# Kernel optimization log

Measured on AMD Instinct MI355X. Metric: run time of the kernel, lower is better.

Reference implementation:

```python
import jax, jax.numpy as jnp
import numpy as np

N = 100000
FEAT = 256
HID = 128
OUT = 64
E = 1600000


def setup_inputs() -> dict:
    key = jax.random.key(0)
    ks = jax.random.split(key, 8)
    x = jax.random.normal(ks[0], (N, FEAT), dtype=jnp.float32)
    edge_index = jax.random.randint(ks[1], (2, E), 0, N, dtype=jnp.int64)
    # Glorot-like weights, zero bias (PyG GCNConv default init style)
    def glorot(k, fin, fout):
        s = (6.0 / (fin + fout)) ** 0.5
        return jax.random.uniform(k, (fin, fout), jnp.float32, -s, s)
    return {
        "x": x,
        "edge_index": edge_index,
        "W1": glorot(ks[2], FEAT, HID), "b1": jnp.zeros((HID,), jnp.float32),
        "W2": glorot(ks[3], HID, HID), "b2": jnp.zeros((HID,), jnp.float32),
        "W3": glorot(ks[4], HID, OUT), "b3": jnp.zeros((OUT,), jnp.float32),
    }


def _gcn_prep(edge_index, n_nodes):
    # Add self-loops and compute symmetric normalization deg^-1/2 (PyG gcn_norm).
    loops = jnp.arange(n_nodes, dtype=edge_index.dtype)
    src = jnp.concatenate([edge_index[0], loops])
    dst = jnp.concatenate([edge_index[1], loops])
    ones = jnp.ones(src.shape[0], dtype=jnp.float32)
    deg = jax.ops.segment_sum(ones, dst, num_segments=n_nodes)
    dinv = jnp.where(deg > 0, jax.lax.rsqrt(jnp.maximum(deg, 1.0)), 0.0)
    norm = dinv[src] * dinv[dst]  # [E+N]
    return src, dst, norm


def _gcn_layer(x, src, dst, norm, W, b, n_nodes):
    h = x @ W                              # [N, F_out]
    msg = h[src] * norm[:, None]           # gather + edge scale
    out = jax.ops.segment_sum(msg, dst, num_segments=n_nodes)  # scatter-add
    return out + b


def reference(x, edge_index, W1, b1, W2, b2, W3, b3):
    n = x.shape[0]
    src, dst, norm = _gcn_prep(edge_index, n)
    h = jax.nn.relu(_gcn_layer(x, src, dst, norm, W1, b1, n))
    h = jax.nn.relu(_gcn_layer(h, src, dst, norm, W2, b2, n))
    return _gcn_layer(h, src, dst, norm, W3, b3, n)
```

## Files before the change

kernel.cpp:

```cpp
#include <hip/hip_runtime.h>
#include <hip/hip_bf16.h>


#define NNODES 100000
#define NB 391
#define PB 2048
#define BCAP 12288

typedef _Float16 half8  __attribute__((ext_vector_type(8)));
typedef _Float16 half4v __attribute__((ext_vector_type(4)));
typedef _Float16 half2v __attribute__((ext_vector_type(2)));
typedef float    floatx4 __attribute__((ext_vector_type(4)));

static __device__ __forceinline__ floatx4 h2f4(half4v v) {
    return (floatx4){(float)v.x, (float)v.y, (float)v.z, (float)v.w};
}

__global__ __launch_bounds__(256) void blockhist_k(const int* __restrict__ dst,
                                                   int* __restrict__ H, int e) {
    __shared__ int h[NB];
    for (int q = threadIdx.x; q < NB; q += 256) h[q] = 0;
    __syncthreads();
    int base = blockIdx.x * PB;
    int lim = e - base; if (lim > PB) lim = PB;
    for (int i = threadIdx.x; i < lim; i += 256)
        atomicAdd(&h[dst[base + i] >> 8], 1);
    __syncthreads();
    for (int q = threadIdx.x; q < NB; q += 256)
        H[(size_t)blockIdx.x * NB + q] = h[q];
}

__global__ __launch_bounds__(256) void bucketscan_k(const int* __restrict__ H,
                                                    int* __restrict__ O,
                                                    int* __restrict__ T, int npb) {
    __shared__ int lds[256];
    int b = blockIdx.x, t = threadIdx.x;
    int running = 0;
    for (int c0 = 0; c0 < npb; c0 += 256) {
        int idx = c0 + t;
        int v = (idx < npb) ? H[(size_t)idx * NB + b] : 0;
        lds[t] = v;
        __syncthreads();
        #pragma unroll
        for (int off = 1; off < 256; off <<= 1) {
            int u = (t >= off) ? lds[t - off] : 0;
            __syncthreads();
            lds[t] += u;
            __syncthreads();
        }
        int excl = lds[t] - v + running;
        if (idx < npb) O[(size_t)idx * NB + b] = excl;
        running += lds[255];
        __syncthreads();
    }
    if (t == 0) T[b] = running;
}

__global__ __launch_bounds__(512) void scanT_k(const int* __restrict__ T,
                                               int* __restrict__ bbase, int e) {
    __shared__ int lds[512];
    int t = threadIdx.x;
    int v = (t < NB) ? T[t] : 0;
    lds[t] = v;
    __syncthreads();
    #pragma unroll
    for (int off = 1; off < 512; off <<= 1) {
        int u = (t >= off) ? lds[t - off] : 0;
        __syncthreads();
        lds[t] += u;
        __syncthreads();
    }
    if (t < NB) bbase[t] = lds[t] - v;
    if (t == 0) bbase[NB] = e;
}

__global__ __launch_bounds__(256) void scatter_k(const int* __restrict__ src,
                                                 const int* __restrict__ dst,
                                                 const int* __restrict__ O,
                                                 const int* __restrict__ bbase,
                                                 unsigned* __restrict__ binned, int e) {
    __shared__ int cur[NB];
    for (int q = threadIdx.x; q < NB; q += 256)
        cur[q] = bbase[q] + O[(size_t)blockIdx.x * NB + q];
    __syncthreads();
    int base = blockIdx.x * PB;
    int lim = e - base; if (lim > PB) lim = PB;
    for (int i = threadIdx.x; i < lim; i += 256) {
        int d = dst[base + i];
        int s = src[base + i];
        int p = atomicAdd(&cur[d >> 8], 1);
        binned[p] = ((unsigned)(d & 255) << 17) | (unsigned)s;
    }
}

__global__ __launch_bounds__(256) void bucket_fill_k(
    const unsigned* __restrict__ binned, const int* __restrict__ bbase,
    int* __restrict__ rowptr, int* __restrict__ eidx,
    float* __restrict__ dinv, int n, int e) {
    __shared__ int cnt[256];
    __shared__ int cur[256];
    __shared__ int lds[256];
    __shared__ int sbuf[BCAP];
    int b = blockIdx.x, t = threadIdx.x;
    int beg = bbase[b], end = bbase[b + 1];
    int m = end - beg;
    cnt[t] = 0;
    __syncthreads();
    for (int q = t; q < m; q += 256) {
        unsigned r = binned[beg + q];
        atomicAdd(&cnt[r >> 17], 1);
    }
    __syncthreads();
    int v = cnt[t];
    lds[t] = v;
    __syncthreads();
    #pragma unroll
    for (int off = 1; off < 256; off <<= 1) {
        int u = (t >= off) ? lds[t - off] : 0;
        __syncthreads();
        lds[t] += u;
        __syncthreads();
    }
    int excl = lds[t] - v;
    int node = b * 256 + t;
    if (node < n) {
        rowptr[node] = beg + excl;
        dinv[node] = rsqrtf(1.0f + (float)v);
    }
    if (b == NB - 1 && t == 0) rowptr[n] = e;
    cur[t] = excl;
    __syncthreads();
    for (int q = t; q < m; q += 256) {
        unsigned r = binned[beg + q];
        int p = atomicAdd(&cur[r >> 17], 1);
        if (p < BCAP) sbuf[p] = (int)(r & 0x1FFFFu);
    }
    __syncthreads();
    for (int q = t; q < m; q += 256) eidx[beg + q] = sbuf[q];
}

static __device__ __forceinline__ void cast_frag(
    const float* __restrict__ W, _Float16* __restrict__ Wf,
    int FIN, int FOUT, int i) {
    int k = i / FOUT, n = i % FOUT;
    int ct = n >> 4, mrow = n & 15;
    int kc = k >> 5, hi = (k & 31) >> 3, j = k & 7;
    int NKC = FIN / 32;
    int idx = ((ct * NKC + kc) * 64 + hi * 16 + mrow) * 8 + j;
    Wf[idx] = (_Float16)W[(size_t)k * FOUT + n];
}

__global__ __launch_bounds__(256) void castW_k(
    const float* __restrict__ W1, const float* __restrict__ W2,
    const float* __restrict__ W3, _Float16* __restrict__ Wf1,
    _Float16* __restrict__ Wf2, _Float16* __restrict__ Wf3) {
    int i = blockIdx.x * 256 + threadIdx.x;
    if (i < 256 * 128) cast_frag(W1, Wf1, 256, 128, i);
    if (i < 128 * 128) cast_frag(W2, Wf2, 128, 128, i);
    if (i < 128 * 64)  cast_frag(W3, Wf3, 128, 64, i);
}

template<typename TA, int FIN, int FOUT>
__global__ __launch_bounds__(256, 2) void gemm_ldsB_k(
    const TA* __restrict__ X, const _Float16* __restrict__ Wf,
    const float* __restrict__ dinv, _Float16* __restrict__ G, int n)
{
    constexpr int NKC = FIN / 32;
    constexpr int NCT = FOUT / 16;
    __shared__ _Float16 wS[FOUT * FIN];

    const int tid  = threadIdx.x;
    const int wave = tid >> 6;
    const int lane = tid & 63;
    const int mrow = lane & 15;
    const int kq   = (lane >> 4) * 8;

    {
        const half8* s = (const half8*)Wf;
        half8* d = (half8*)wS;
        constexpr int TOT8 = FOUT * FIN / 8;
        #pragma unroll
        for (int i = tid; i < TOT8; i += 256) d[i] = s[i];
    }

    int r = blockIdx.x * 64 + wave * 16 + mrow;
    if (r > n - 1) r = n - 1;

    half8 af[NKC];
    if constexpr (sizeof(TA) == 4) {
        const float* xp = (const float*)X + (size_t)r * FIN + kq;
        float4 t0[NKC], t1[NKC];
        #pragma unroll
        for (int kc = 0; kc < NKC; ++kc) {
            t0[kc] = *(const float4*)(xp + kc * 32);
            t1[kc] = *(const float4*)(xp + kc * 32 + 4);
        }
        #pragma unroll
        for (int kc = 0; kc < NKC; ++kc) {
            float4 u0 = t0[kc], u1 = t1[kc];
            af[kc] = (half8){(_Float16)u0.x, (_Float16)u0.y, (_Float16)u0.z, (_Float16)u0.w,
                             (_Float16)u1.x, (_Float16)u1.y, (_Float16)u1.z, (_Float16)u1.w};
        }
    } else {
        const _Float16* xp = (const _Float16*)X + (size_t)r * FIN + kq;
        #pragma unroll
        for (int kc = 0; kc < NKC; ++kc)
            af[kc] = *(const half8*)(xp + kc * 32);
    }

    __syncthreads();

    floatx4 acc[NCT];
    #pragma unroll
    for (int ct = 0; ct < NCT; ++ct) acc[ct] = (floatx4){0.f, 0.f, 0.f, 0.f};

    #pragma unroll
    for (int kc = 0; kc < NKC; ++kc) {
        #pragma unroll
        for (int ct = 0; ct < NCT; ++ct) {
            half8 bf = *(const half8*)&wS[(((ct * NKC) + kc) * 64 + lane) * 8];
            acc[ct] = __builtin_amdgcn_mfma_f32_16x16x32_f16(af[kc], bf, acc[ct], 0, 0, 0);
        }
    }

    int rbase = blockIdx.x * 64 + wave * 16 + (lane >> 4) * 4;
    #pragma unroll
    for (int reg = 0; reg < 4; ++reg) {
        int rr = rbase + reg;
        if (rr < n) {
            float s = dinv[rr];
            #pragma unroll
            for (int ct = 0; ct < NCT; ++ct)
                G[(size_t)rr * FOUT + ct * 16 + mrow] = (_Float16)(acc[ct][reg] * s);
        }
    }
}

template<bool RELU, typename OutT>
__global__ __launch_bounds__(256) void gather128_k(
    const _Float16* __restrict__ g, const int* __restrict__ rowptr,
    const int* __restrict__ eidx, const float* __restrict__ dinv,
    const float* __restrict__ bias, OutT* __restrict__ out, int n)
{
    int wave = threadIdx.x >> 6;
    int lane = threadIdx.x & 63;
    int half = lane >> 5;
    int hl   = lane & 31;
    int node = blockIdx.x * 4 + wave;
    if (node >= n) return;

    int beg = rowptr[node];
    int end = rowptr[node + 1];

    const half4v* g4 = (const half4v*)g;
    floatx4 aA = {0.f,0.f,0.f,0.f}, aB = aA, aC = aA, aD = aA;
    if (half == 0) aA = h2f4(g4[(size_t)node * 32 + hl]);

    for (int j0 = beg; j0 < end; j0 += 64) {
        int m = end - j0; if (m > 64) m = 64;
        int id = (lane < m) ? eidx[j0 + lane] : 0;
        int t = 0;
        for (; t + 7 < m; t += 8) {
            int i0 = __shfl(id, t + half);
            int i1 = __shfl(id, t + 2 + half);
            int i2 = __shfl(id, t + 4 + half);
            int i3 = __shfl(id, t + 6 + half);
            half4v v0 = g4[(size_t)i0 * 32 + hl];
            half4v v1 = g4[(size_t)i1 * 32 + hl];
            half4v v2 = g4[(size_t)i2 * 32 + hl];
            half4v v3 = g4[(size_t)i3 * 32 + hl];
            aA += h2f4(v0); aB += h2f4(v1); aC += h2f4(v2); aD += h2f4(v3);
        }
        for (; t + 1 < m; t += 2) {
            int i0 = __shfl(id, t + half);
            aA += h2f4(g4[(size_t)i0 * 32 + hl]);
        }
        if (t < m) {
            int i0 = __shfl(id, t);
            if (half == 0) aA += h2f4(g4[(size_t)i0 * 32 + hl]);
        }
    }
    aA += aB; aC += aD; aA += aC;
    aA.x += __shfl_down(aA.x, 32);
    aA.y += __shfl_down(aA.y, 32);
    aA.z += __shfl_down(aA.z, 32);
    aA.w += __shfl_down(aA.w, 32);

    if (half == 0) {
        float sc = dinv[node];
        float4 bb = *(const float4*)(bias + 4 * hl);
        float o0 = fmaf(aA.x, sc, bb.x);
        float o1 = fmaf(aA.y, sc, bb.y);
        float o2 = fmaf(aA.z, sc, bb.z);
        float o3 = fmaf(aA.w, sc, bb.w);
        if (RELU) {
            o0 = fmaxf(o0, 0.f); o1 = fmaxf(o1, 0.f);
            o2 = fmaxf(o2, 0.f); o3 = fmaxf(o3, 0.f);
        }
        if constexpr (sizeof(OutT) == 2) {
            ((half4v*)out)[(size_t)node * 32 + hl] =
                (half4v){(_Float16)o0, (_Float16)o1, (_Float16)o2, (_Float16)o3};
        } else {
            *(float4*)((float*)out + (size_t)node * 128 + 4 * hl) =
                make_float4(o0, o1, o2, o3);
        }
    }
}

template<bool RELU>
__global__ __launch_bounds__(256) void gather64_k(
    const _Float16* __restrict__ g, const int* __restrict__ rowptr,
    const int* __restrict__ eidx, const float* __restrict__ dinv,
    const float* __restrict__ bias, float* __restrict__ out, int n)
{
    int wave = threadIdx.x >> 6;
    int lane = threadIdx.x & 63;
    int half = lane >> 5;
    int hl   = lane & 31;
    int node = blockIdx.x * 4 + wave;
    if (node >= n) return;

    int beg = rowptr[node];
    int end = rowptr[node + 1];

    const half2v* g2 = (const half2v*)g;
    float ax=0.f, ay=0.f, bx=0.f, by=0.f, cx=0.f, cy=0.f, dx=0.f, dy=0.f;
    if (half == 0) {
        half2v v = g2[(size_t)node * 32 + hl];
        ax = (float)v.x; ay = (float)v.y;
    }

    for (int j0 = beg; j0 < end; j0 += 64) {
        int m = end - j0; if (m > 64) m = 64;
        int id = (lane < m) ? eidx[j0 + lane] : 0;
        int t = 0;
        for (; t + 7 < m; t += 8) {
            int i0 = __shfl(id, t + half);
            int i1 = __shfl(id, t + 2 + half);
            int i2 = __shfl(id, t + 4 + half);
            int i3 = __shfl(id, t + 6 + half);
            half2v v0 = g2[(size_t)i0 * 32 + hl];
            half2v v1 = g2[(size_t)i1 * 32 + hl];
            half2v v2 = g2[(size_t)i2 * 32 + hl];
            half2v v3 = g2[(size_t)i3 * 32 + hl];
            ax += (float)v0.x; ay += (float)v0.y;
            bx += (float)v1.x; by += (float)v1.y;
            cx += (float)v2.x; cy += (float)v2.y;
            dx += (float)v3.x; dy += (float)v3.y;
        }
        for (; t + 1 < m; t += 2) {
            int i0 = __shfl(id, t + half);
            half2v v0 = g2[(size_t)i0 * 32 + hl];
            ax += (float)v0.x; ay += (float)v0.y;
        }
        if (t < m) {
            int i0 = __shfl(id, t);
            if (half == 0) {
                half2v v0 = g2[(size_t)i0 * 32 + hl];
                ax += (float)v0.x; ay += (float)v0.y;
            }
        }
    }
    ax += bx + cx + dx; ay += by + cy + dy;
    ax += __shfl_down(ax, 32);
    ay += __shfl_down(ay, 32);

    if (half == 0) {
        float sc = dinv[node];
        float2 bb = *(const float2*)(bias + 2 * hl);
        float ox = fmaf(ax, sc, bb.x);
        float oy = fmaf(ay, sc, bb.y);
        if (RELU) { ox = fmaxf(ox, 0.f); oy = fmaxf(oy, 0.f); }
        *(float2*)(out + (size_t)node * 64 + 2 * hl) = make_float2(ox, oy);
    }
}

extern "C" void kernel_launch(void* const* d_in, const int* in_sizes, int n_in,
                              void* d_out, int out_size, void* d_ws, size_t ws_size,
                              hipStream_t stream) {
    const float* x  = (const float*)d_in[0];
    const int*   ei = (const int*)d_in[1];
    const float* W1 = (const float*)d_in[2];
    const float* b1 = (const float*)d_in[3];
    const float* W2 = (const float*)d_in[4];
    const float* b2 = (const float*)d_in[5];
    const float* W3 = (const float*)d_in[6];
    const float* b3 = (const float*)d_in[7];
    float* out = (float*)d_out;

    const int N = NNODES;
    const int E = in_sizes[1] / 2;
    const int* srcI = ei;
    const int* dstI = ei + E;

    const int npb = (E + PB - 1) / PB;

    char* ws = (char*)d_ws;
    size_t p = 0;
    auto alloc = [&](size_t bytes) { void* r = ws + p; p = (p + bytes + 255) & ~(size_t)255; return r; };
    float*     dinv   = (float*)    alloc((size_t)N * 4);
    int*       rowptr = (int*)      alloc((size_t)(N + 1) * 4);
    int*       bbase  = (int*)      alloc((size_t)(NB + 1) * 4);
    int*       T      = (int*)      alloc((size_t)NB * 4);
    int*       H      = (int*)      alloc((size_t)npb * NB * 4);
    int*       O      = (int*)      alloc((size_t)npb * NB * 4);
    unsigned*  binned = (unsigned*) alloc((size_t)E * 4);
    int*       eidx   = (int*)      alloc((size_t)E * 4);
    _Float16*  Wf1    = (_Float16*) alloc((size_t)128 * 256 * 2);
    _Float16*  Wf2    = (_Float16*) alloc((size_t)128 * 128 * 2);
    _Float16*  Wf3    = (_Float16*) alloc((size_t)64 * 128 * 2);
    _Float16*  A      = (_Float16*) alloc((size_t)N * 128 * 2);
    _Float16*  Ch     = (_Float16*) alloc((size_t)N * 128 * 2);

    const int nb_node4 = (N + 3) / 4;
    const int nb_gemm = (N + 63) / 64;

    blockhist_k<<<npb, 256, 0, stream>>>(dstI, H, E);
    castW_k<<<128, 256, 0, stream>>>(W1, W2, W3, Wf1, Wf2, Wf3);
    bucketscan_k<<<NB, 256, 0, stream>>>(H, O, T, npb);
    scanT_k<<<1, 512, 0, stream>>>(T, bbase, E);
    scatter_k<<<npb, 256, 0, stream>>>(srcI, dstI, O, bbase, binned, E);
    bucket_fill_k<<<NB, 256, 0, stream>>>(binned, bbase, rowptr, eidx, dinv, N, E);

    gemm_ldsB_k<float, 256, 128><<<nb_gemm, 256, 0, stream>>>(x, Wf1, dinv, A, N);
    gather128_k<true, _Float16><<<nb_node4, 256, 0, stream>>>(A, rowptr, eidx, dinv, b1, Ch, N);

    gemm_ldsB_k<_Float16, 128, 128><<<nb_gemm, 256, 0, stream>>>(Ch, Wf2, dinv, A, N);
    gather128_k<true, _Float16><<<nb_node4, 256, 0, stream>>>(A, rowptr, eidx, dinv, b2, Ch, N);

    gemm_ldsB_k<_Float16, 128, 64><<<nb_gemm, 256, 0, stream>>>(Ch, Wf3, dinv, A, N);
    gather64_k<false><<<nb_node4, 256, 0, stream>>>(A, rowptr, eidx, dinv, b3, out, N);
}
```

Measured before the change: 445.3 us.

## Store features in 16-column chunk-major layout and gather per chunk

The GEMM output and the gather input/output switch from row-major to a chunk-major layout, with 16 half-precision columns per chunk and every node contiguous within a chunk. Each gather block handles a single chunk, so the working set of gathered rows (N×32 bytes) is small enough to stay cache-resident across random neighbour accesses. A quarter-wave now processes one node, loading 16 edge indices at a time and reducing with xor shuffles. In exchange, edge indices and rowptr are read once per chunk (8×) instead of once in total, and partial edge batches waste lanes.

```diff
diff --git a/kernel.cpp b/kernel.cpp
--- a/kernel.cpp
+++ b/kernel.cpp
@@ -9,7 +9,6 @@
 
 typedef _Float16 half8  __attribute__((ext_vector_type(8)));
 typedef _Float16 half4v __attribute__((ext_vector_type(4)));
-typedef _Float16 half2v __attribute__((ext_vector_type(2)));
 typedef float    floatx4 __attribute__((ext_vector_type(4)));
 
 static __device__ __forceinline__ floatx4 h2f4(half4v v) {
@@ -202,10 +201,12 @@
                              (_Float16)u1.x, (_Float16)u1.y, (_Float16)u1.z, (_Float16)u1.w};
         }
     } else {
-        const _Float16* xp = (const _Float16*)X + (size_t)r * FIN + kq;
-        #pragma unroll
-        for (int kc = 0; kc < NKC; ++kc)
-            af[kc] = *(const half8*)(xp + kc * 32);
+        const _Float16* xp = (const _Float16*)X;
+        #pragma unroll
+        for (int kc = 0; kc < NKC; ++kc) {
+            int f0 = kc * 32 + kq;
+            af[kc] = *(const half8*)(xp + ((size_t)(f0 >> 4) * n + r) * 16 + (f0 & 15));
+        }
     }
 
     __syncthreads();
@@ -231,147 +232,89 @@
             float s = dinv[rr];
             #pragma unroll
             for (int ct = 0; ct < NCT; ++ct)
-                G[(size_t)rr * FOUT + ct * 16 + mrow] = (_Float16)(acc[ct][reg] * s);
-        }
-    }
-}
-
-template<bool RELU, typename OutT>
-__global__ __launch_bounds__(256) void gather128_k(
+                G[((size_t)ct * n + rr) * 16 + mrow] = (_Float16)(acc[ct][reg] * s);
+        }
+    }
+}
+
+template<int NCHUNK, bool RELU, bool F32OUT>
+__global__ __launch_bounds__(256) void gatherchunk_k(
     const _Float16* __restrict__ g, const int* __restrict__ rowptr,
     const int* __restrict__ eidx, const float* __restrict__ dinv,
-    const float* __restrict__ bias, OutT* __restrict__ out, int n)
+    const float* __restrict__ bias, void* __restrict__ outv, int n)
 {
-    int wave = threadIdx.x >> 6;
-    int lane = threadIdx.x & 63;
-    int half = lane >> 5;
-    int hl   = lane & 31;
-    int node = blockIdx.x * 4 + wave;
-    if (node >= n) return;
-
-    int beg = rowptr[node];
-    int end = rowptr[node + 1];
-
-    const half4v* g4 = (const half4v*)g;
-    floatx4 aA = {0.f,0.f,0.f,0.f}, aB = aA, aC = aA, aD = aA;
-    if (half == 0) aA = h2f4(g4[(size_t)node * 32 + hl]);
-
-    for (int j0 = beg; j0 < end; j0 += 64) {
-        int m = end - j0; if (m > 64) m = 64;
-        int id = (lane < m) ? eidx[j0 + lane] : 0;
-        int t = 0;
-        for (; t + 7 < m; t += 8) {
-            int i0 = __shfl(id, t + half);
-            int i1 = __shfl(id, t + 2 + half);
-            int i2 = __shfl(id, t + 4 + half);
-            int i3 = __shfl(id, t + 6 + half);
-            half4v v0 = g4[(size_t)i0 * 32 + hl];
-            half4v v1 = g4[(size_t)i1 * 32 + hl];
-            half4v v2 = g4[(size_t)i2 * 32 + hl];
-            half4v v3 = g4[(size_t)i3 * 32 + hl];
-            aA += h2f4(v0); aB += h2f4(v1); aC += h2f4(v2); aD += h2f4(v3);
-        }
-        for (; t + 1 < m; t += 2) {
-            int i0 = __shfl(id, t + half);
-            aA += h2f4(g4[(size_t)i0 * 32 + hl]);
-        }
-        if (t < m) {
-            int i0 = __shfl(id, t);
-            if (half == 0) aA += h2f4(g4[(size_t)i0 * 32 + hl]);
-        }
-    }
-    aA += aB; aC += aD; aA += aC;
-    aA.x += __shfl_down(aA.x, 32);
-    aA.y += __shfl_down(aA.y, 32);
-    aA.z += __shfl_down(aA.z, 32);
-    aA.w += __shfl_down(aA.w, 32);
-
-    if (half == 0) {
-        float sc = dinv[node];
-        float4 bb = *(const float4*)(bias + 4 * hl);
-        float o0 = fmaf(aA.x, sc, bb.x);
-        float o1 = fmaf(aA.y, sc, bb.y);
-        float o2 = fmaf(aA.z, sc, bb.z);
-        float o3 = fmaf(aA.w, sc, bb.w);
+    const int lane    = threadIdx.x & 63;
+    const int wave    = threadIdx.x >> 6;
+    const int quarter = lane >> 4;
+    const int ql      = lane & 15;
+    const int grp     = ql >> 2;
+    const int q       = ql & 3;
+
+    const int cg = blockIdx.x & 7;
+    const int nb = blockIdx.x >> 3;
+    int chunk, n0, nlim;
+    if constexpr (NCHUNK == 8) {
+        chunk = cg; n0 = 0; nlim = n;
+    } else {
+        chunk = cg & 3;
+        int hh = (n + 1) >> 1;
+        n0   = (cg >> 2) ? hh : 0;
+        nlim = (cg >> 2) ? n  : hh;
+    }
+    const _Float16* __restrict__ gc = g + (size_t)chunk * n * 16;
+    const float4 bb = *(const float4*)(bias + chunk * 16 + 4 * q);
+
+    const int node = n0 + nb * 16 + wave * 4 + quarter;
+    if (node >= nlim) return;
+
+    const int beg = rowptr[node];
+    const int end = rowptr[node + 1];
+    const float sc = dinv[node];
+
+    floatx4 acc = {0.f, 0.f, 0.f, 0.f};
+    {
+        half4v v = *(const half4v*)(gc + ((node << 4) | (q << 2)));
+        if (grp == 0) acc = h2f4(v);
+    }
+
+    for (int j0 = beg; j0 < end; j0 += 16) {
+        int m = end - j0; if (m > 16) m = 16;
+        int id = (ql < m) ? __builtin_nontemporal_load(eidx + j0 + ql) : 0;
+        #pragma unroll
+        for (int t = 0; t < 16; t += 4) {
+            int e = t + grp;
+            int src = __shfl(id, (lane & 48) + e);
+            half4v v = *(const half4v*)(gc + ((src << 4) | (q << 2)));
+            if (e < m) acc += h2f4(v);
+        }
+    }
+
+    #pragma unroll
+    for (int off = 4; off <= 8; off <<= 1) {
+        acc.x += __shfl_xor(acc.x, off);
+        acc.y += __shfl_xor(acc.y, off);
+        acc.z += __shfl_xor(acc.z, off);
+        acc.w += __shfl_xor(acc.w, off);
+    }
+
+    if (grp == 0) {
+        float o0 = fmaf(acc.x, sc, bb.x);
+        float o1 = fmaf(acc.y, sc, bb.y);
+        float o2 = fmaf(acc.z, sc, bb.z);
+        float o3 = fmaf(acc.w, sc, bb.w);
         if (RELU) {
             o0 = fmaxf(o0, 0.f); o1 = fmaxf(o1, 0.f);
             o2 = fmaxf(o2, 0.f); o3 = fmaxf(o3, 0.f);
         }
-        if constexpr (sizeof(OutT) == 2) {
-            ((half4v*)out)[(size_t)node * 32 + hl] =
-                (half4v){(_Float16)o0, (_Float16)o1, (_Float16)o2, (_Float16)o3};
+        if constexpr (F32OUT) {
+            floatx4* p = (floatx4*)((float*)outv + (size_t)node * (NCHUNK * 16)
+                                    + chunk * 16 + 4 * q);
+            __builtin_nontemporal_store((floatx4){o0, o1, o2, o3}, p);
         } else {
-            *(float4*)((float*)out + (size_t)node * 128 + 4 * hl) =
-                make_float4(o0, o1, o2, o3);
-        }
-    }
-}
-
-template<bool RELU>
-__global__ __launch_bounds__(256) void gather64_k(
-    const _Float16* __restrict__ g, const int* __restrict__ rowptr,
-    const int* __restrict__ eidx, const float* __restrict__ dinv,
-    const float* __restrict__ bias, float* __restrict__ out, int n)
-{
-    int wave = threadIdx.x >> 6;
-    int lane = threadIdx.x & 63;
-    int half = lane >> 5;
-    int hl   = lane & 31;
-    int node = blockIdx.x * 4 + wave;
-    if (node >= n) return;
-
-    int beg = rowptr[node];
-    int end = rowptr[node + 1];
-
-    const half2v* g2 = (const half2v*)g;
-    float ax=0.f, ay=0.f, bx=0.f, by=0.f, cx=0.f, cy=0.f, dx=0.f, dy=0.f;
-    if (half == 0) {
-        half2v v = g2[(size_t)node * 32 + hl];
-        ax = (float)v.x; ay = (float)v.y;
-    }
-
-    for (int j0 = beg; j0 < end; j0 += 64) {
-        int m = end - j0; if (m > 64) m = 64;
-        int id = (lane < m) ? eidx[j0 + lane] : 0;
-        int t = 0;
-        for (; t + 7 < m; t += 8) {
-            int i0 = __shfl(id, t + half);
-            int i1 = __shfl(id, t + 2 + half);
-            int i2 = __shfl(id, t + 4 + half);
-            int i3 = __shfl(id, t + 6 + half);
-            half2v v0 = g2[(size_t)i0 * 32 + hl];
-            half2v v1 = g2[(size_t)i1 * 32 + hl];
-            half2v v2 = g2[(size_t)i2 * 32 + hl];
-            half2v v3 = g2[(size_t)i3 * 32 + hl];
-            ax += (float)v0.x; ay += (float)v0.y;
-            bx += (float)v1.x; by += (float)v1.y;
-            cx += (float)v2.x; cy += (float)v2.y;
-            dx += (float)v3.x; dy += (float)v3.y;
-        }
-        for (; t + 1 < m; t += 2) {
-            int i0 = __shfl(id, t + half);
-            half2v v0 = g2[(size_t)i0 * 32 + hl];
-            ax += (float)v0.x; ay += (float)v0.y;
-        }
-        if (t < m) {
-            int i0 = __shfl(id, t);
-            if (half == 0) {
-                half2v v0 = g2[(size_t)i0 * 32 + hl];
-                ax += (float)v0.x; ay += (float)v0.y;
-            }
-        }
-    }
-    ax += bx + cx + dx; ay += by + cy + dy;
-    ax += __shfl_down(ax, 32);
-    ay += __shfl_down(ay, 32);
-
-    if (half == 0) {
-        float sc = dinv[node];
-        float2 bb = *(const float2*)(bias + 2 * hl);
-        float ox = fmaf(ax, sc, bb.x);
-        float oy = fmaf(ay, sc, bb.y);
-        if (RELU) { ox = fmaxf(ox, 0.f); oy = fmaxf(oy, 0.f); }
-        *(float2*)(out + (size_t)node * 64 + 2 * hl) = make_float2(ox, oy);
+            half4v hv = {(_Float16)o0, (_Float16)o1, (_Float16)o2, (_Float16)o3};
+            half4v* p = (half4v*)outv + ((size_t)chunk * n + node) * 4 + q;
+            __builtin_nontemporal_store(hv, p);
+        }
     }
 }
 
@@ -412,8 +355,9 @@
     _Float16*  A      = (_Float16*) alloc((size_t)N * 128 * 2);
     _Float16*  Ch     = (_Float16*) alloc((size_t)N * 128 * 2);
 
-    const int nb_node4 = (N + 3) / 4;
-    const int nb_gemm = (N + 63) / 64;
+    const int nb_gemm  = (N + 63) / 64;
+    const int nb_gc128 = ((N + 15) / 16) * 8;
+    const int nb_gc64  = (((N + 1) / 2 + 15) / 16) * 8;
 
     blockhist_k<<<npb, 256, 0, stream>>>(dstI, H, E);
     castW_k<<<128, 256, 0, stream>>>(W1, W2, W3, Wf1, Wf2, Wf3);
@@ -423,11 +367,11 @@
     bucket_fill_k<<<NB, 256, 0, stream>>>(binned, bbase, rowptr, eidx, dinv, N, E);
 
     gemm_ldsB_k<float, 256, 128><<<nb_gemm, 256, 0, stream>>>(x, Wf1, dinv, A, N);
-    gather128_k<true, _Float16><<<nb_node4, 256, 0, stream>>>(A, rowptr, eidx, dinv, b1, Ch, N);
+    gatherchunk_k<8, true, false><<<nb_gc128, 256, 0, stream>>>(A, rowptr, eidx, dinv, b1, Ch, N);
 
     gemm_ldsB_k<_Float16, 128, 128><<<nb_gemm, 256, 0, stream>>>(Ch, Wf2, dinv, A, N);
-    gather128_k<true, _Float16><<<nb_node4, 256, 0, stream>>>(A, rowptr, eidx, dinv, b2, Ch, N);
+    gatherchunk_k<8, true, false><<<nb_gc128, 256, 0, stream>>>(A, rowptr, eidx, dinv, b2, Ch, N);
 
     gemm_ldsB_k<_Float16, 128, 64><<<nb_gemm, 256, 0, stream>>>(Ch, Wf3, dinv, A, N);
-    gather64_k<false><<<nb_node4, 256, 0, stream>>>(A, rowptr, eidx, dinv, b3, out, N);
-}
+    gatherchunk_k<4, false, true><<<nb_gc64, 256, 0, stream>>>(A, rowptr, eidx, dinv, b3, out, N);
+}
```

Result: slower. 606.2 us (+36.1%).

## Stream GEMM weights from global with register double-buffering; nontemporal gather IO

Applied to the files above, without the earlier changes.

The GEMM kernel no longer stages the whole weight matrix in LDS behind a block barrier. Each wave now loads its B fragments straight from global memory (expected to hit L2/L1) into two register buffers, prefetching the next k-chunk while MFMAs run on the current one. This removes the LDS fill, the __syncthreads and the LDS occupancy limit, at the cost of redundant global weight reads per wave and higher register pressure. The gather kernels also switch to nontemporal loads of edge indices and nontemporal stores of outputs to reduce cache pollution.

```diff
diff --git a/kernel.cpp b/kernel.cpp
--- a/kernel.cpp
+++ b/kernel.cpp
@@ -161,13 +161,12 @@
 }
 
 template<typename TA, int FIN, int FOUT>
-__global__ __launch_bounds__(256, 2) void gemm_ldsB_k(
+__global__ __launch_bounds__(256) void gemm_pipe_k(
     const TA* __restrict__ X, const _Float16* __restrict__ Wf,
     const float* __restrict__ dinv, _Float16* __restrict__ G, int n)
 {
     constexpr int NKC = FIN / 32;
     constexpr int NCT = FOUT / 16;
-    __shared__ _Float16 wS[FOUT * FIN];
 
     const int tid  = threadIdx.x;
     const int wave = tid >> 6;
@@ -175,14 +174,6 @@
     const int mrow = lane & 15;
     const int kq   = (lane >> 4) * 8;
 
-    {
-        const half8* s = (const half8*)Wf;
-        half8* d = (half8*)wS;
-        constexpr int TOT8 = FOUT * FIN / 8;
-        #pragma unroll
-        for (int i = tid; i < TOT8; i += 256) d[i] = s[i];
-    }
-
     int r = blockIdx.x * 64 + wave * 16 + mrow;
     if (r > n - 1) r = n - 1;
 
@@ -208,19 +199,34 @@
             af[kc] = *(const half8*)(xp + kc * 32);
     }
 
-    __syncthreads();
-
     floatx4 acc[NCT];
     #pragma unroll
     for (int ct = 0; ct < NCT; ++ct) acc[ct] = (floatx4){0.f, 0.f, 0.f, 0.f};
 
-    #pragma unroll
-    for (int kc = 0; kc < NKC; ++kc) {
-        #pragma unroll
-        for (int ct = 0; ct < NCT; ++ct) {
-            half8 bf = *(const half8*)&wS[(((ct * NKC) + kc) * 64 + lane) * 8];
-            acc[ct] = __builtin_amdgcn_mfma_f32_16x16x32_f16(af[kc], bf, acc[ct], 0, 0, 0);
-        }
+    const half8* bfp = (const half8*)Wf;
+    half8 bfA[NCT], bfB[NCT];
+
+    #pragma unroll
+    for (int ct = 0; ct < NCT; ++ct)
+        bfA[ct] = bfp[(size_t)(ct * NKC) * 64 + lane];
+
+    #pragma unroll
+    for (int kc2 = 0; kc2 < NKC; kc2 += 2) {
+        #pragma unroll
+        for (int ct = 0; ct < NCT; ++ct)
+            bfB[ct] = bfp[(size_t)(ct * NKC + kc2 + 1) * 64 + lane];
+        #pragma unroll
+        for (int ct = 0; ct < NCT; ++ct)
+            acc[ct] = __builtin_amdgcn_mfma_f32_16x16x32_f16(af[kc2], bfA[ct], acc[ct], 0, 0, 0);
+
+        if (kc2 + 2 < NKC) {
+            #pragma unroll
+            for (int ct = 0; ct < NCT; ++ct)
+                bfA[ct] = bfp[(size_t)(ct * NKC + kc2 + 2) * 64 + lane];
+        }
+        #pragma unroll
+        for (int ct = 0; ct < NCT; ++ct)
+            acc[ct] = __builtin_amdgcn_mfma_f32_16x16x32_f16(af[kc2 + 1], bfB[ct], acc[ct], 0, 0, 0);
     }
 
     int rbase = blockIdx.x * 64 + wave * 16 + (lane >> 4) * 4;
@@ -258,7 +264,7 @@
 
     for (int j0 = beg; j0 < end; j0 += 64) {
         int m = end - j0; if (m > 64) m = 64;
-        int id = (lane < m) ? eidx[j0 + lane] : 0;
+        int id = (lane < m) ? __builtin_nontemporal_load(eidx + j0 + lane) : 0;
         int t = 0;
         for (; t + 7 < m; t += 8) {
             int i0 = __shfl(id, t + half);
@@ -298,11 +304,12 @@
             o2 = fmaxf(o2, 0.f); o3 = fmaxf(o3, 0.f);
         }
         if constexpr (sizeof(OutT) == 2) {
-            ((half4v*)out)[(size_t)node * 32 + hl] =
-                (half4v){(_Float16)o0, (_Float16)o1, (_Float16)o2, (_Float16)o3};
+            half4v hv = {(_Float16)o0, (_Float16)o1, (_Float16)o2, (_Float16)o3};
+            __builtin_nontemporal_store(hv, (half4v*)out + (size_t)node * 32 + hl);
         } else {
-            *(float4*)((float*)out + (size_t)node * 128 + 4 * hl) =
-                make_float4(o0, o1, o2, o3);
+            __builtin_nontemporal_store(
+                (floatx4){o0, o1, o2, o3},
+                (floatx4*)((float*)out + (size_t)node * 128 + 4 * hl));
         }
     }
 }
@@ -332,7 +339,7 @@
 
     for (int j0 = beg; j0 < end; j0 += 64) {
         int m = end - j0; if (m > 64) m = 64;
-        int id = (lane < m) ? eidx[j0 + lane] : 0;
+        int id = (lane < m) ? __builtin_nontemporal_load(eidx + j0 + lane) : 0;
         int t = 0;
         for (; t + 7 < m; t += 8) {
             int i0 = __shfl(id, t + half);
@@ -413,7 +420,7 @@
     _Float16*  Ch     = (_Float16*) alloc((size_t)N * 128 * 2);
 
     const int nb_node4 = (N + 3) / 4;
-    const int nb_gemm = (N + 63) / 64;
+    const int nb_gemm  = (N + 63) / 64;
 
     blockhist_k<<<npb, 256, 0, stream>>>(dstI, H, E);
     castW_k<<<128, 256, 0, stream>>>(W1, W2, W3, Wf1, Wf2, Wf3);
@@ -422,12 +429,12 @@
     scatter_k<<<npb, 256, 0, stream>>>(srcI, dstI, O, bbase, binned, E);
     bucket_fill_k<<<NB, 256, 0, stream>>>(binned, bbase, rowptr, eidx, dinv, N, E);
 
-    gemm_ldsB_k<float, 256, 128><<<nb_gemm, 256, 0, stream>>>(x, Wf1, dinv, A, N);
+    gemm_pipe_k<float, 256, 128><<<nb_gemm, 256, 0, stream>>>(x, Wf1, dinv, A, N);
     gather128_k<true, _Float16><<<nb_node4, 256, 0, stream>>>(A, rowptr, eidx, dinv, b1, Ch, N);
 
-    gemm_ldsB_k<_Float16, 128, 128><<<nb_gemm, 256, 0, stream>>>(Ch, Wf2, dinv, A, N);
+    gemm_pipe_k<_Float16, 128, 128><<<nb_gemm, 256, 0, stream>>>(Ch, Wf2, dinv, A, N);
     gather128_k<true, _Float16><<<nb_node4, 256, 0, stream>>>(A, rowptr, eidx, dinv, b2, Ch, N);
 
-    gemm_ldsB_k<_Float16, 128, 64><<<nb_gemm, 256, 0, stream>>>(Ch, Wf3, dinv, A, N);
+    gemm_pipe_k<_Float16, 128, 64><<<nb_gemm, 256, 0, stream>>>(Ch, Wf3, dinv, A, N);
     gather64_k<false><<<nb_node4, 256, 0, stream>>>(A, rowptr, eidx, dinv, b3, out, N);
 }
```

Result: slower. 460.6 us (+3.4%).
